# Performance work log

Hardware: AMD Instinct MI355X
Metric: run time of the kernel (lower is better)

Reference implementation:

```python
import jax, jax.numpy as jnp
import numpy as np

H = 1024        # hidden_size
E = 8           # num_experts
K = 2           # experts_per_token
I = 1024        # intermediate_size (mlp1 outputs 2*I, interleaved gate/linear)
N = 4096        # n_tokens
ALPHA = 1.702
LIMIT = 7.0
EPS = 1e-5


def setup_inputs() -> dict:
    key = jax.random.key(0)
    ks = jax.random.split(key, 5)
    x = jax.random.normal(ks[0], (N, H), jnp.float32)
    norm_scale = jnp.ones((H,), jnp.float32)
    gate_w = jax.random.normal(ks[1], (H, E), jnp.float32) * 0.02
    gate_b = jnp.zeros((E,), jnp.float32)
    mlp1_w = jax.random.normal(ks[2], (E, 2 * I, H), jnp.float32) * 0.02
    mlp1_b = jnp.zeros((E, 2 * I), jnp.float32)
    mlp2_w = jax.random.normal(ks[3], (E, H, I), jnp.float32) * 0.02
    mlp2_b = jnp.zeros((E, H), jnp.float32)
    return {"x": x, "norm_scale": norm_scale, "gate_w": gate_w, "gate_b": gate_b,
            "mlp1_w": mlp1_w, "mlp1_b": mlp1_b, "mlp2_w": mlp2_w, "mlp2_b": mlp2_b}


def _swiglu(h):
    # even indices = gate, odd indices = linear (interleaved)
    x_g = jnp.minimum(h[..., ::2], LIMIT)           # clip gate above only
    x_l = jnp.clip(h[..., 1::2], -LIMIT, LIMIT)     # clip linear both sides
    return x_g * jax.nn.sigmoid(ALPHA * x_g) * (x_l + 1.0)


def reference(x, norm_scale, gate_w, gate_b, mlp1_w, mlp1_b, mlp2_w, mlp2_b):
    # RMSNorm (fp32)
    t = x * jax.lax.rsqrt(jnp.mean(x * x, axis=-1, keepdims=True) + EPS) * norm_scale
    # Router: top-k gating with softmax over selected logits
    g = t @ gate_w + gate_b                          # [N, E]
    logits, idx = jax.lax.top_k(g, K)                # [N, K]
    w = jax.nn.softmax(logits, axis=-1)              # [N, K]
    n = x.shape[0]
    # Scatter routing weights into dense combine matrix [N, E]
    # (top_k indices are unique per row, so .set is exact)
    combine = jnp.zeros((n, E), x.dtype).at[jnp.arange(n)[:, None], idx].set(w)
    # Per-expert SwiGLU MLP over all tokens, weighted combine + residual.
    # Loop over the small fixed expert count (E=8); avoids materializing the
    # huge [N, K, 2I, H] gathered-weight tensor from the original gather path.
    out = x
    for e in range(E):
        h1 = _swiglu(t @ mlp1_w[e].T + mlp1_b[e])    # [N, I]
        h2 = h1 @ mlp2_w[e].T + mlp2_b[e]            # [N, H]
        out = out + combine[:, e:e + 1] * h2
    return out
```

## Files before the change

kernel.cpp:

```cpp
#include <hip/hip_runtime.h>
#include <hip/hip_bf16.h>
#include <stdint.h>

#define HDIM 1024
#define NEXP 8
#define TOPK 2
#define IDIM 1024
#define TWO_I 2048
#define ALPHA 1.702f
#define LIMIT 7.0f
#define EPS 1e-5f

#define BM 128
#define BN 128
#define BK 64

typedef __attribute__((ext_vector_type(8))) short bf16x8;
typedef __attribute__((ext_vector_type(4))) float f32x4;

typedef __attribute__((address_space(1))) const uint32_t g_u32;
typedef __attribute__((address_space(3))) uint32_t l_u32;

__device__ __forceinline__ void load_lds16(const void* g, void* l) {
    __builtin_amdgcn_global_load_lds((g_u32*)g, (l_u32*)l, 16, 0, 0);
}

__device__ __forceinline__ ushort f2bf(float f) {
    union { float f; uint32_t u; } v{f};
    uint32_t u = v.u;
    return (ushort)((u + 0x7fffu + ((u >> 16) & 1u)) >> 16);
}

#define WAIT_VM8()  do { asm volatile("s_waitcnt vmcnt(8)" ::: "memory"); \
                         __builtin_amdgcn_sched_barrier(0); } while (0)
#define WAIT_VM0()  do { asm volatile("s_waitcnt vmcnt(0)" ::: "memory"); \
                         __builtin_amdgcn_sched_barrier(0); } while (0)
#define BAR()       do { __builtin_amdgcn_sched_barrier(0); \
                         __builtin_amdgcn_s_barrier(); \
                         __builtin_amdgcn_sched_barrier(0); } while (0)

__global__ __launch_bounds__(256) void k_f32_to_bf16(const float* __restrict__ src,
                                                     ushort* __restrict__ dst, int n4) {
    int i = blockIdx.x * blockDim.x + threadIdx.x;
    int stride = gridDim.x * blockDim.x;
    for (; i < n4; i += stride) {
        float4 v = reinterpret_cast<const float4*>(src)[i];
        ushort4 o;
        o.x = f2bf(v.x); o.y = f2bf(v.y); o.z = f2bf(v.z); o.w = f2bf(v.w);
        reinterpret_cast<ushort4*>(dst)[i] = o;
    }
}

__global__ __launch_bounds__(256) void k_conv_w1(const float* __restrict__ src,
                                                 ushort* __restrict__ dst) {
    const int b = blockIdx.x;
    const int e = b >> 11;
    const int j = b & 2047;
    const int dj = ((j & 1) << 10) | (j >> 1);
    const float4* s = reinterpret_cast<const float4*>(src + (size_t)b * HDIM);
    ushort4* d = reinterpret_cast<ushort4*>(dst + ((size_t)e * TWO_I + dj) * HDIM);
    float4 v = s[threadIdx.x];
    ushort4 o;
    o.x = f2bf(v.x); o.y = f2bf(v.y); o.z = f2bf(v.z); o.w = f2bf(v.w);
    d[threadIdx.x] = o;
}

__global__ __launch_bounds__(256) void k_norm_gate(
    const float* __restrict__ x, const float* __restrict__ scale,
    const float* __restrict__ gw, const float* __restrict__ gb,
    ushort* __restrict__ t_bf, float* __restrict__ route_w,
    int* __restrict__ eidx, int n_tok)
{
    const int tok = blockIdx.x * 4 + (threadIdx.x >> 6);
    if (tok >= n_tok) return;
    const int lane = threadIdx.x & 63;

    const float4* xr = reinterpret_cast<const float4*>(x + (size_t)tok * HDIM);
    const float4* sr = reinterpret_cast<const float4*>(scale);
    float4 xv[4], sv[4];
    #pragma unroll
    for (int j = 0; j < 4; ++j) { xv[j] = xr[lane + 64 * j]; sv[j] = sr[lane + 64 * j]; }

    float ss = 0.f;
    #pragma unroll
    for (int j = 0; j < 4; ++j)
        ss += xv[j].x * xv[j].x + xv[j].y * xv[j].y + xv[j].z * xv[j].z + xv[j].w * xv[j].w;
    #pragma unroll
    for (int off = 1; off < 64; off <<= 1) ss += __shfl_xor(ss, off, 64);
    const float rms = rsqrtf(ss / (float)HDIM + EPS);

    float t[4][4];
    ushort4* tw = reinterpret_cast<ushort4*>(t_bf + (size_t)tok * HDIM);
    #pragma unroll
    for (int j = 0; j < 4; ++j) {
        t[j][0] = xv[j].x * rms * sv[j].x;
        t[j][1] = xv[j].y * rms * sv[j].y;
        t[j][2] = xv[j].z * rms * sv[j].z;
        t[j][3] = xv[j].w * rms * sv[j].w;
        ushort4 o;
        o.x = f2bf(t[j][0]); o.y = f2bf(t[j][1]); o.z = f2bf(t[j][2]); o.w = f2bf(t[j][3]);
        tw[lane + 64 * j] = o;
    }

    float g[NEXP];
    #pragma unroll
    for (int e = 0; e < NEXP; ++e) g[e] = 0.f;
    const float4* gwv = reinterpret_cast<const float4*>(gw);
    #pragma unroll
    for (int j = 0; j < 4; ++j) {
        #pragma unroll
        for (int c = 0; c < 4; ++c) {
            const int h = (lane + 64 * j) * 4 + c;
            const float tv = t[j][c];
            const float4 a = gwv[h * 2 + 0];
            const float4 b = gwv[h * 2 + 1];
            g[0] += tv * a.x; g[1] += tv * a.y; g[2] += tv * a.z; g[3] += tv * a.w;
            g[4] += tv * b.x; g[5] += tv * b.y; g[6] += tv * b.z; g[7] += tv * b.w;
        }
    }
    #pragma unroll
    for (int e = 0; e < NEXP; ++e) {
        #pragma unroll
        for (int off = 1; off < 64; off <<= 1) g[e] += __shfl_xor(g[e], off, 64);
    }

    if (lane == 0) {
        float gg[NEXP];
        #pragma unroll
        for (int e = 0; e < NEXP; ++e) gg[e] = g[e] + gb[e];
        int i0 = 0; float l0 = gg[0];
        #pragma unroll
        for (int e = 1; e < NEXP; ++e) if (gg[e] > l0) { l0 = gg[e]; i0 = e; }
        int i1 = -1; float l1 = -3.4e38f;
        #pragma unroll
        for (int e = 0; e < NEXP; ++e) if (e != i0 && gg[e] > l1) { l1 = gg[e]; i1 = e; }
        const float w0 = 1.f / (1.f + __expf(l1 - l0));
        route_w[tok * 2 + 0] = w0;
        route_w[tok * 2 + 1] = 1.f - w0;
        eidx[tok * 2 + 0] = i0;
        eidx[tok * 2 + 1] = i1;
    }
}

#define BKT_BLOCKS 8
__global__ __launch_bounds__(256) void k_bucket(
    const int* __restrict__ eidx, int* __restrict__ counts,
    int* __restrict__ bucket, int n_tok)
{
    const int total = 2 * n_tok;
    const int per_block = total / BKT_BLOCKS;
    const int rounds = per_block / 256;
    const int base_ent = blockIdx.x * per_block;
    const int tid = threadIdx.x;
    const int lane = tid & 63, wid = tid >> 6;

    __shared__ int wavecnt[4][4][NEXP];
    __shared__ int cum[4][4][NEXP];
    __shared__ int gbase[NEXP];

    int me[4], rank[4];
    #pragma unroll
    for (int r = 0; r < 4; ++r) {
        const int ent = base_ent + r * 256 + tid;
        const int e = (r < rounds) ? eidx[ent] : -1;
        me[r] = e;
        #pragma unroll
        for (int ex = 0; ex < NEXP; ++ex) {
            unsigned long long m = __ballot(e == ex);
            if (e == ex) rank[r] = __popcll(m & ((1ull << lane) - 1ull));
            if (lane == 0) wavecnt[r][wid][ex] = (int)__popcll(m);
        }
    }
    __syncthreads();

    if (tid < 4 * 4 * NEXP) {
        const int e = tid & 7, w = (tid >> 3) & 3, r = tid >> 5;
        int s = 0;
        for (int rr = 0; rr < 4; ++rr)
            for (int ww = 0; ww < 4; ++ww)
                if (rr < r || (rr == r && ww < w)) s += wavecnt[rr][ww][e];
        cum[r][w][e] = s;
    }
    __syncthreads();
    if (tid < NEXP) {
        int tot = 0;
        for (int rr = 0; rr < 4; ++rr)
            for (int ww = 0; ww < 4; ++ww) tot += wavecnt[rr][ww][tid];
        gbase[tid] = atomicAdd(&counts[tid], tot);
    }
    __syncthreads();

    #pragma unroll
    for (int r = 0; r < 4; ++r) {
        const int e = me[r];
        if (e >= 0) {
            const int ent = base_ent + r * 256 + tid;
            bucket[e * n_tok + gbase[e] + cum[r][wid][e] + rank[r]] = ent;
        }
    }
}

__global__ __launch_bounds__(256) void k_gemm1(
    const ushort* __restrict__ tA, const ushort* __restrict__ w1bf,
    const float* __restrict__ b1,
    const int* __restrict__ counts, const int* __restrict__ bucket,
    ushort* __restrict__ h1, int n_tok, int rt_max)
{
    const int bx = blockIdx.x;
    const int rt = bx >> 7;
    const int e  = (bx >> 4) & 7;
    const int jt = bx & 15;
    const int cnt = counts[e];
    if (rt * BM >= cnt) return;

    __shared__ __align__(16) ushort As[2][BM * BK];
    __shared__ __align__(16) ushort Bs[2][BN * BK];

    const int tid = threadIdx.x;
    const int lane = tid & 63, wid = tid >> 6;
    const int wm = wid >> 1, wn = wid & 1;

    int tokrow[4];
    #pragma unroll
    for (int it = 0; it < 4; ++it) {
        int pos = rt * BM + it * 32 + (tid >> 3);
        tokrow[it] = bucket[e * n_tok + min(pos, cnt - 1)] >> 1;
    }
    const ushort* wbase = w1bf + (size_t)e * TWO_I * HDIM;
    const ushort* bsrc[4];
    #pragma unroll
    for (int it = 0; it < 4; ++it) {
        int br = it * 32 + (tid >> 3);
        int G = br >> 4, r16 = br & 15;
        int half = (G >> 1) & 1;
        int sub = ((G >> 2) << 1) | (G & 1);
        int srcrow = half * IDIM + jt * 64 + sub * 16 + r16;
        bsrc[it] = wbase + (size_t)srcrow * HDIM;
    }
    const int swz = (((tid & 7) ^ ((tid >> 3) & 7)) * 8);

    f32x4 acc[4][4];
    #pragma unroll
    for (int mi = 0; mi < 4; ++mi)
        #pragma unroll
        for (int ni = 0; ni < 4; ++ni) acc[mi][ni] = (f32x4)0.f;

    auto stage = [&](int buf, int kt) {
        const int k0 = kt * BK + swz;
        #pragma unroll
        for (int it = 0; it < 4; ++it)
            load_lds16(tA + (size_t)tokrow[it] * HDIM + k0, &As[buf][(it * 32 + wid * 8) * BK]);
        #pragma unroll
        for (int it = 0; it < 4; ++it)
            load_lds16(bsrc[it] + k0, &Bs[buf][(it * 32 + wid * 8) * BK]);
    };
    auto compute = [&](int buf) {
        #pragma unroll
        for (int kk = 0; kk < 2; ++kk) {
            bf16x8 a[4], b[4];
            #pragma unroll
            for (int mi = 0; mi < 4; ++mi) {
                int r = wm * 64 + mi * 16 + (lane & 15);
                int off = r * BK + (((kk * 4 + (lane >> 4)) ^ (lane & 7)) * 8);
                a[mi] = *reinterpret_cast<const bf16x8*>(&As[buf][off]);
            }
            #pragma unroll
            for (int ni = 0; ni < 4; ++ni) {
                int r = wn * 64 + ni * 16 + (lane & 15);
                int off = r * BK + (((kk * 4 + (lane >> 4)) ^ (lane & 7)) * 8);
                b[ni] = *reinterpret_cast<const bf16x8*>(&Bs[buf][off]);
            }
            #pragma unroll
            for (int mi = 0; mi < 4; ++mi)
                #pragma unroll
                for (int ni = 0; ni < 4; ++ni)
                    acc[mi][ni] = __builtin_amdgcn_mfma_f32_16x16x32_bf16(a[mi], b[ni], acc[mi][ni], 0, 0, 0);
        }
    };

    stage(0, 0);
    int cur = 0;
    for (int kt = 0; kt < HDIM / BK - 1; ++kt) {
        stage(cur ^ 1, kt + 1);
        WAIT_VM8();
        BAR();
        compute(cur);
        BAR();
        cur ^= 1;
    }
    WAIT_VM0();
    BAR();
    compute(cur);

    int ent[4][4];
    #pragma unroll
    for (int mi = 0; mi < 4; ++mi)
        #pragma unroll
        for (int r = 0; r < 4; ++r) {
            int pos = rt * BM + wm * 64 + mi * 16 + (lane >> 4) * 4 + r;
            ent[mi][r] = (pos < cnt) ? bucket[e * n_tok + pos] : -1;
        }
    #pragma unroll
    for (int ni = 0; ni < 2; ++ni) {
        const int col = jt * 64 + (wn * 2 + ni) * 16 + (lane & 15);
        const float bg = b1[e * TWO_I + 2 * col];
        const float bl = b1[e * TWO_I + 2 * col + 1];
        #pragma unroll
        for (int mi = 0; mi < 4; ++mi) {
            const f32x4 vg = acc[mi][ni];
            const f32x4 vl = acc[mi][ni + 2];
            #pragma unroll
            for (int r = 0; r < 4; ++r) {
                if (ent[mi][r] >= 0) {
                    const float xg = fminf(vg[r] + bg, LIMIT);
                    const float xl = fminf(fmaxf(vl[r] + bl, -LIMIT), LIMIT);
                    const float s = 1.f / (1.f + __expf(-ALPHA * xg));
                    h1[(size_t)ent[mi][r] * IDIM + col] = f2bf(xg * s * (xl + 1.f));
                }
            }
        }
    }
}

__global__ __launch_bounds__(256) void k_gemm2(
    const ushort* __restrict__ h1, const ushort* __restrict__ w2bf,
    const float* __restrict__ b2, const float* __restrict__ route_w,
    const int* __restrict__ counts, const int* __restrict__ bucket,
    float* __restrict__ contrib, int n_tok, int rt_max)
{
    const int bx = blockIdx.x;
    const int rt = bx >> 6;
    const int e  = (bx >> 3) & 7;
    const int ct = bx & 7;
    const int cnt = counts[e];
    if (rt * BM >= cnt) return;
    const int c0 = ct * BN;

    __shared__ __align__(16) ushort As[2][BM * BK];
    __shared__ __align__(16) ushort Bs[2][BN * BK];

    const int tid = threadIdx.x;
    const int lane = tid & 63, wid = tid >> 6;
    const int wm = wid >> 1, wn = wid & 1;

    int rowent[4];
    #pragma unroll
    for (int it = 0; it < 4; ++it) {
        int pos = rt * BM + it * 32 + (tid >> 3);
        rowent[it] = bucket[e * n_tok + min(pos, cnt - 1)];
    }
    const ushort* wB = w2bf + (size_t)e * HDIM * IDIM;
    const int swz = (((tid & 7) ^ ((tid >> 3) & 7)) * 8);

    f32x4 acc[4][4];
    #pragma unroll
    for (int mi = 0; mi < 4; ++mi)
        #pragma unroll
        for (int ni = 0; ni < 4; ++ni) acc[mi][ni] = (f32x4)0.f;

    auto stage = [&](int buf, int kt) {
        const int k0 = kt * BK + swz;
        #pragma unroll
        for (int it = 0; it < 4; ++it)
            load_lds16(h1 + (size_t)rowent[it] * IDIM + k0, &As[buf][(it * 32 + wid * 8) * BK]);
        #pragma unroll
        for (int it = 0; it < 4; ++it)
            load_lds16(wB + (size_t)(c0 + it * 32 + (tid >> 3)) * IDIM + k0, &Bs[buf][(it * 32 + wid * 8) * BK]);
    };
    auto compute = [&](int buf) {
        #pragma unroll
        for (int kk = 0; kk < 2; ++kk) {
            bf16x8 a[4], b[4];
            #pragma unroll
            for (int mi = 0; mi < 4; ++mi) {
                int r = wm * 64 + mi * 16 + (lane & 15);
                int off = r * BK + (((kk * 4 + (lane >> 4)) ^ (lane & 7)) * 8);
                a[mi] = *reinterpret_cast<const bf16x8*>(&As[buf][off]);
            }
            #pragma unroll
            for (int ni = 0; ni < 4; ++ni) {
                int r = wn * 64 + ni * 16 + (lane & 15);
                int off = r * BK + (((kk * 4 + (lane >> 4)) ^ (lane & 7)) * 8);
                b[ni] = *reinterpret_cast<const bf16x8*>(&Bs[buf][off]);
            }
            #pragma unroll
            for (int mi = 0; mi < 4; ++mi)
                #pragma unroll
                for (int ni = 0; ni < 4; ++ni)
                    acc[mi][ni] = __builtin_amdgcn_mfma_f32_16x16x32_bf16(a[mi], b[ni], acc[mi][ni], 0, 0, 0);
        }
    };

    stage(0, 0);
    int cur = 0;
    for (int kt = 0; kt < IDIM / BK - 1; ++kt) {
        stage(cur ^ 1, kt + 1);
        WAIT_VM8();
        BAR();
        compute(cur);
        BAR();
        cur ^= 1;
    }
    WAIT_VM0();
    BAR();
    compute(cur);

    int ent[4][4];
    float wgt[4][4];
    #pragma unroll
    for (int mi = 0; mi < 4; ++mi)
        #pragma unroll
        for (int r = 0; r < 4; ++r) {
            int pos = rt * BM + wm * 64 + mi * 16 + (lane >> 4) * 4 + r;
            if (pos < cnt) {
                ent[mi][r] = bucket[e * n_tok + pos];
                wgt[mi][r] = route_w[ent[mi][r]];
            } else ent[mi][r] = -1;
        }
    #pragma unroll
    for (int ni = 0; ni < 4; ++ni) {
        const int c = c0 + wn * 64 + ni * 16 + (lane & 15);
        const float bc = b2[e * HDIM + c];
        #pragma unroll
        for (int mi = 0; mi < 4; ++mi) {
            const f32x4 v = acc[mi][ni];
            #pragma unroll
            for (int r = 0; r < 4; ++r) {
                if (ent[mi][r] >= 0) {
                    const int tok = ent[mi][r] >> 1, slot = ent[mi][r] & 1;
                    contrib[((size_t)slot * n_tok + tok) * HDIM + c] = wgt[mi][r] * (v[r] + bc);
                }
            }
        }
    }
}

__global__ __launch_bounds__(256) void k_combine(
    const float* __restrict__ x, const float* __restrict__ contrib,
    float* __restrict__ out, int n4, int slot_stride4)
{
    int i = blockIdx.x * blockDim.x + threadIdx.x;
    if (i >= n4) return;
    float4 xv = reinterpret_cast<const float4*>(x)[i];
    float4 c0 = reinterpret_cast<const float4*>(contrib)[i];
    float4 c1 = reinterpret_cast<const float4*>(contrib)[i + slot_stride4];
    float4 o;
    o.x = xv.x + c0.x + c1.x;
    o.y = xv.y + c0.y + c1.y;
    o.z = xv.z + c0.z + c1.z;
    o.w = xv.w + c0.w + c1.w;
    reinterpret_cast<float4*>(out)[i] = o;
}

extern "C" void kernel_launch(void* const* d_in, const int* in_sizes, int n_in,
                              void* d_out, int out_size, void* d_ws, size_t ws_size,
                              hipStream_t stream) {
    const float* x    = (const float*)d_in[0];
    const float* nsc  = (const float*)d_in[1];
    const float* gw   = (const float*)d_in[2];
    const float* gb   = (const float*)d_in[3];
    const float* w1   = (const float*)d_in[4];
    const float* b1   = (const float*)d_in[5];
    const float* w2   = (const float*)d_in[6];
    const float* b2   = (const float*)d_in[7];
    float* out = (float*)d_out;

    const int N = in_sizes[0] / HDIM;
    const int rt_max = (N + BM - 1) / BM;

    uintptr_t p = (uintptr_t)d_ws;
    auto carve = [&p](size_t bytes) { uintptr_t q = p; p += (bytes + 255) & ~(size_t)255; return q; };
    ushort* t_bf    = (ushort*)carve((size_t)N * HDIM * 2);
    ushort* w1bf    = (ushort*)carve((size_t)NEXP * TWO_I * HDIM * 2);
    ushort* w2bf    = (ushort*)carve((size_t)NEXP * HDIM * IDIM * 2);
    ushort* h1      = (ushort*)carve((size_t)N * TOPK * IDIM * 2);
    float*  contrib = (float*)carve((size_t)TOPK * N * HDIM * 4);
    float*  route_w = (float*)carve((size_t)N * TOPK * 4);
    int*    bucket  = (int*)carve((size_t)NEXP * N * 4);
    int*    eidx    = (int*)carve((size_t)N * TOPK * 4);
    int*    counts  = (int*)carve(256);

    hipMemsetAsync(counts, 0, NEXP * sizeof(int), stream);

    k_conv_w1<<<NEXP * TWO_I, 256, 0, stream>>>(w1, w1bf);
    const int n4w2 = NEXP * HDIM * IDIM / 4;
    k_f32_to_bf16<<<2048, 256, 0, stream>>>(w2, w2bf, n4w2);

    k_norm_gate<<<(N + 3) / 4, 256, 0, stream>>>(x, nsc, gw, gb, t_bf, route_w, eidx, N);
    k_bucket<<<BKT_BLOCKS, 256, 0, stream>>>(eidx, counts, bucket, N);

    k_gemm1<<<rt_max * NEXP * (TWO_I / BN), 256, 0, stream>>>(t_bf, w1bf, b1, counts, bucket, h1, N, rt_max);
    k_gemm2<<<rt_max * NEXP * (HDIM / BN), 256, 0, stream>>>(h1, w2bf, b2, route_w, counts, bucket, contrib, N, rt_max);

    const int n4 = N * HDIM / 4;
    k_combine<<<(n4 + 255) / 256, 256, 0, stream>>>(x, contrib, out, n4, n4);
}
```

Baseline: 328.0 us.

## Enlarge gemm1 tiles to 256x256 with 8 waves and add XCD block swizzle

The first expert GEMM moves from 128x128 tiles with 4 waves to 256x256 tiles with 8 waves per block, which raises arithmetic intensity per LDS load and halves the number of weight and activation reloads. Both expert GEMMs also remap block IDs with an XCD swizzle so that neighbouring tiles sharing the same expert weights land on the same chiplet's L2. The cost is heavier register and LDS use per block (64 KB LDS, 128 accumulator floats per thread), fewer blocks, and more padding waste when per-expert token counts are not multiples of 256.

```diff
diff --git a/kernel.cpp b/kernel.cpp
--- a/kernel.cpp
+++ b/kernel.cpp
@@ -11,8 +11,6 @@
 #define LIMIT 7.0f
 #define EPS 1e-5f
 
-#define BM 128
-#define BN 128
 #define BK 64
 
 typedef __attribute__((ext_vector_type(8))) short bf16x8;
@@ -38,6 +36,11 @@
 #define BAR()       do { __builtin_amdgcn_sched_barrier(0); \
                          __builtin_amdgcn_s_barrier(); \
                          __builtin_amdgcn_sched_barrier(0); } while (0)
+
+__device__ __forceinline__ int xcd_swizzle(int bid, int nwg) {
+    const int cpx = nwg >> 3;
+    return (bid & 7) * cpx + (bid >> 3);
+}
 
 __global__ __launch_bounds__(256) void k_f32_to_bf16(const float* __restrict__ src,
                                                      ushort* __restrict__ dst, int n4) {
@@ -200,48 +203,48 @@
     }
 }
 
-__global__ __launch_bounds__(256) void k_gemm1(
+#define G1_BM 256
+#define G1_BN 256
+__global__ __launch_bounds__(512, 2) void k_gemm1(
     const ushort* __restrict__ tA, const ushort* __restrict__ w1bf,
     const float* __restrict__ b1,
     const int* __restrict__ counts, const int* __restrict__ bucket,
-    ushort* __restrict__ h1, int n_tok, int rt_max)
+    ushort* __restrict__ h1, int n_tok, int nwg)
 {
-    const int bx = blockIdx.x;
-    const int rt = bx >> 7;
-    const int e  = (bx >> 4) & 7;
-    const int jt = bx & 15;
+    const int bx = xcd_swizzle(blockIdx.x, nwg);
+    const int rt = bx >> 6;
+    const int e  = (bx >> 3) & 7;
+    const int jt = bx & 7;
     const int cnt = counts[e];
-    if (rt * BM >= cnt) return;
-
-    __shared__ __align__(16) ushort As[2][BM * BK];
-    __shared__ __align__(16) ushort Bs[2][BN * BK];
+    if (rt * G1_BM >= cnt) return;
+
+    __shared__ __align__(16) ushort As[2][G1_BM * BK];
+    __shared__ __align__(16) ushort Bs[2][G1_BN * BK];
 
     const int tid = threadIdx.x;
     const int lane = tid & 63, wid = tid >> 6;
-    const int wm = wid >> 1, wn = wid & 1;
+    const int wm = wid >> 2, wn = wid & 3;
 
     int tokrow[4];
     #pragma unroll
     for (int it = 0; it < 4; ++it) {
-        int pos = rt * BM + it * 32 + (tid >> 3);
+        int pos = rt * G1_BM + it * 64 + (tid >> 3);
         tokrow[it] = bucket[e * n_tok + min(pos, cnt - 1)] >> 1;
     }
     const ushort* wbase = w1bf + (size_t)e * TWO_I * HDIM;
     const ushort* bsrc[4];
     #pragma unroll
     for (int it = 0; it < 4; ++it) {
-        int br = it * 32 + (tid >> 3);
-        int G = br >> 4, r16 = br & 15;
-        int half = (G >> 1) & 1;
-        int sub = ((G >> 2) << 1) | (G & 1);
-        int srcrow = half * IDIM + jt * 64 + sub * 16 + r16;
+        int br = it * 64 + (tid >> 3);
+        int wnb = br >> 6, q = (br >> 4) & 3, r16 = br & 15;
+        int srcrow = ((q >> 1) ? IDIM : 0) + jt * 128 + wnb * 32 + (q & 1) * 16 + r16;
         bsrc[it] = wbase + (size_t)srcrow * HDIM;
     }
     const int swz = (((tid & 7) ^ ((tid >> 3) & 7)) * 8);
 
-    f32x4 acc[4][4];
-    #pragma unroll
-    for (int mi = 0; mi < 4; ++mi)
+    f32x4 acc[8][4];
+    #pragma unroll
+    for (int mi = 0; mi < 8; ++mi)
         #pragma unroll
         for (int ni = 0; ni < 4; ++ni) acc[mi][ni] = (f32x4)0.f;
 
@@ -249,18 +252,18 @@
         const int k0 = kt * BK + swz;
         #pragma unroll
         for (int it = 0; it < 4; ++it)
-            load_lds16(tA + (size_t)tokrow[it] * HDIM + k0, &As[buf][(it * 32 + wid * 8) * BK]);
+            load_lds16(tA + (size_t)tokrow[it] * HDIM + k0, &As[buf][(it * 64 + wid * 8) * BK]);
         #pragma unroll
         for (int it = 0; it < 4; ++it)
-            load_lds16(bsrc[it] + k0, &Bs[buf][(it * 32 + wid * 8) * BK]);
+            load_lds16(bsrc[it] + k0, &Bs[buf][(it * 64 + wid * 8) * BK]);
     };
     auto compute = [&](int buf) {
         #pragma unroll
         for (int kk = 0; kk < 2; ++kk) {
-            bf16x8 a[4], b[4];
-            #pragma unroll
-            for (int mi = 0; mi < 4; ++mi) {
-                int r = wm * 64 + mi * 16 + (lane & 15);
+            bf16x8 a[8], b[4];
+            #pragma unroll
+            for (int mi = 0; mi < 8; ++mi) {
+                int r = wm * 128 + mi * 16 + (lane & 15);
                 int off = r * BK + (((kk * 4 + (lane >> 4)) ^ (lane & 7)) * 8);
                 a[mi] = *reinterpret_cast<const bf16x8*>(&As[buf][off]);
             }
@@ -271,7 +274,7 @@
                 b[ni] = *reinterpret_cast<const bf16x8*>(&Bs[buf][off]);
             }
             #pragma unroll
-            for (int mi = 0; mi < 4; ++mi)
+            for (int mi = 0; mi < 8; ++mi)
                 #pragma unroll
                 for (int ni = 0; ni < 4; ++ni)
                     acc[mi][ni] = __builtin_amdgcn_mfma_f32_16x16x32_bf16(a[mi], b[ni], acc[mi][ni], 0, 0, 0);
@@ -292,21 +295,21 @@
     BAR();
     compute(cur);
 
-    int ent[4][4];
-    #pragma unroll
-    for (int mi = 0; mi < 4; ++mi)
+    int ent[8][4];
+    #pragma unroll
+    for (int mi = 0; mi < 8; ++mi)
         #pragma unroll
         for (int r = 0; r < 4; ++r) {
-            int pos = rt * BM + wm * 64 + mi * 16 + (lane >> 4) * 4 + r;
+            int pos = rt * G1_BM + wm * 128 + mi * 16 + (lane >> 4) * 4 + r;
             ent[mi][r] = (pos < cnt) ? bucket[e * n_tok + pos] : -1;
         }
     #pragma unroll
     for (int ni = 0; ni < 2; ++ni) {
-        const int col = jt * 64 + (wn * 2 + ni) * 16 + (lane & 15);
-        const float bg = b1[e * TWO_I + 2 * col];
-        const float bl = b1[e * TWO_I + 2 * col + 1];
-        #pragma unroll
-        for (int mi = 0; mi < 4; ++mi) {
+        const int icol = jt * 128 + wn * 32 + ni * 16 + (lane & 15);
+        const float bg = b1[e * TWO_I + 2 * icol];
+        const float bl = b1[e * TWO_I + 2 * icol + 1];
+        #pragma unroll
+        for (int mi = 0; mi < 8; ++mi) {
             const f32x4 vg = acc[mi][ni];
             const f32x4 vl = acc[mi][ni + 2];
             #pragma unroll
@@ -315,20 +318,22 @@
                     const float xg = fminf(vg[r] + bg, LIMIT);
                     const float xl = fminf(fmaxf(vl[r] + bl, -LIMIT), LIMIT);
                     const float s = 1.f / (1.f + __expf(-ALPHA * xg));
-                    h1[(size_t)ent[mi][r] * IDIM + col] = f2bf(xg * s * (xl + 1.f));
+                    h1[(size_t)ent[mi][r] * IDIM + icol] = f2bf(xg * s * (xl + 1.f));
                 }
             }
         }
     }
 }
 
+#define BM 128
+#define BN 128
 __global__ __launch_bounds__(256) void k_gemm2(
     const ushort* __restrict__ h1, const ushort* __restrict__ w2bf,
     const float* __restrict__ b2, const float* __restrict__ route_w,
     const int* __restrict__ counts, const int* __restrict__ bucket,
-    float* __restrict__ contrib, int n_tok, int rt_max)
+    float* __restrict__ contrib, int n_tok, int nwg)
 {
-    const int bx = blockIdx.x;
+    const int bx = xcd_swizzle(blockIdx.x, nwg);
     const int rt = bx >> 6;
     const int e  = (bx >> 3) & 7;
     const int ct = bx & 7;
@@ -466,7 +471,6 @@
     float* out = (float*)d_out;
 
     const int N = in_sizes[0] / HDIM;
-    const int rt_max = (N + BM - 1) / BM;
 
     uintptr_t p = (uintptr_t)d_ws;
     auto carve = [&p](size_t bytes) { uintptr_t q = p; p += (bytes + 255) & ~(size_t)255; return q; };
@@ -489,8 +493,13 @@
     k_norm_gate<<<(N + 3) / 4, 256, 0, stream>>>(x, nsc, gw, gb, t_bf, route_w, eidx, N);
     k_bucket<<<BKT_BLOCKS, 256, 0, stream>>>(eidx, counts, bucket, N);
 
-    k_gemm1<<<rt_max * NEXP * (TWO_I / BN), 256, 0, stream>>>(t_bf, w1bf, b1, counts, bucket, h1, N, rt_max);
-    k_gemm2<<<rt_max * NEXP * (HDIM / BN), 256, 0, stream>>>(h1, w2bf, b2, route_w, counts, bucket, contrib, N, rt_max);
+    const int rt1 = (N + G1_BM - 1) / G1_BM;
+    const int nwg1 = rt1 * NEXP * (TWO_I / G1_BN);
+    k_gemm1<<<nwg1, 512, 0, stream>>>(t_bf, w1bf, b1, counts, bucket, h1, N, nwg1);
+
+    const int rt2 = (N + BM - 1) / BM;
+    const int nwg2 = rt2 * NEXP * (HDIM / BN);
+    k_gemm2<<<nwg2, 256, 0, stream>>>(h1, w2bf, b2, route_w, counts, bucket, contrib, N, nwg2);
 
     const int n4 = N * HDIM / 4;
     k_combine<<<(n4 + 255) / 256, 256, 0, stream>>>(x, contrib, out, n4, n4);
```

New measurement: 508.4 us. 55.0% more time.

## Drop LDS double buffering, raise occupancy, and swizzle blocks across XCDs

Applied to the files above, without the earlier changes.

Both grouped GEMM kernels switch from double-buffered LDS staging to a single buffer with a full vmcnt(0) wait each k-step, halving LDS per block. The launch bounds now request 4 blocks per CU, so more workgroups can be resident to hide latency. Block IDs are remapped so consecutive logical tiles land on the same XCD, which should improve L2 reuse of expert weights. The cost is that loads no longer overlap compute within a block, and the swizzle assumes the grid size is divisible by 8.

```diff
diff --git a/kernel.cpp b/kernel.cpp
--- a/kernel.cpp
+++ b/kernel.cpp
@@ -31,13 +31,16 @@
     return (ushort)((u + 0x7fffu + ((u >> 16) & 1u)) >> 16);
 }
 
-#define WAIT_VM8()  do { asm volatile("s_waitcnt vmcnt(8)" ::: "memory"); \
-                         __builtin_amdgcn_sched_barrier(0); } while (0)
 #define WAIT_VM0()  do { asm volatile("s_waitcnt vmcnt(0)" ::: "memory"); \
                          __builtin_amdgcn_sched_barrier(0); } while (0)
 #define BAR()       do { __builtin_amdgcn_sched_barrier(0); \
                          __builtin_amdgcn_s_barrier(); \
                          __builtin_amdgcn_sched_barrier(0); } while (0)
+
+__device__ __forceinline__ int xcd_swizzle(int bid, int nwg) {
+    const int cpx = nwg >> 3;
+    return (bid & 7) * cpx + (bid >> 3);
+}
 
 __global__ __launch_bounds__(256) void k_f32_to_bf16(const float* __restrict__ src,
                                                      ushort* __restrict__ dst, int n4) {
@@ -200,21 +203,21 @@
     }
 }
 
-__global__ __launch_bounds__(256) void k_gemm1(
+__global__ __launch_bounds__(256, 4) void k_gemm1(
     const ushort* __restrict__ tA, const ushort* __restrict__ w1bf,
     const float* __restrict__ b1,
     const int* __restrict__ counts, const int* __restrict__ bucket,
-    ushort* __restrict__ h1, int n_tok, int rt_max)
+    ushort* __restrict__ h1, int n_tok, int nwg)
 {
-    const int bx = blockIdx.x;
+    const int bx = xcd_swizzle(blockIdx.x, nwg);
     const int rt = bx >> 7;
     const int e  = (bx >> 4) & 7;
     const int jt = bx & 15;
     const int cnt = counts[e];
     if (rt * BM >= cnt) return;
 
-    __shared__ __align__(16) ushort As[2][BM * BK];
-    __shared__ __align__(16) ushort Bs[2][BN * BK];
+    __shared__ __align__(16) ushort As[BM * BK];
+    __shared__ __align__(16) ushort Bs[BN * BK];
 
     const int tid = threadIdx.x;
     const int lane = tid & 63, wid = tid >> 6;
@@ -245,16 +248,16 @@
         #pragma unroll
         for (int ni = 0; ni < 4; ++ni) acc[mi][ni] = (f32x4)0.f;
 
-    auto stage = [&](int buf, int kt) {
+    auto stage = [&](int kt) {
         const int k0 = kt * BK + swz;
         #pragma unroll
         for (int it = 0; it < 4; ++it)
-            load_lds16(tA + (size_t)tokrow[it] * HDIM + k0, &As[buf][(it * 32 + wid * 8) * BK]);
+            load_lds16(tA + (size_t)tokrow[it] * HDIM + k0, &As[(it * 32 + wid * 8) * BK]);
         #pragma unroll
         for (int it = 0; it < 4; ++it)
-            load_lds16(bsrc[it] + k0, &Bs[buf][(it * 32 + wid * 8) * BK]);
+            load_lds16(bsrc[it] + k0, &Bs[(it * 32 + wid * 8) * BK]);
     };
-    auto compute = [&](int buf) {
+    auto compute = [&]() {
         #pragma unroll
         for (int kk = 0; kk < 2; ++kk) {
             bf16x8 a[4], b[4];
@@ -262,13 +265,13 @@
             for (int mi = 0; mi < 4; ++mi) {
                 int r = wm * 64 + mi * 16 + (lane & 15);
                 int off = r * BK + (((kk * 4 + (lane >> 4)) ^ (lane & 7)) * 8);
-                a[mi] = *reinterpret_cast<const bf16x8*>(&As[buf][off]);
+                a[mi] = *reinterpret_cast<const bf16x8*>(&As[off]);
             }
             #pragma unroll
             for (int ni = 0; ni < 4; ++ni) {
                 int r = wn * 64 + ni * 16 + (lane & 15);
                 int off = r * BK + (((kk * 4 + (lane >> 4)) ^ (lane & 7)) * 8);
-                b[ni] = *reinterpret_cast<const bf16x8*>(&Bs[buf][off]);
+                b[ni] = *reinterpret_cast<const bf16x8*>(&Bs[off]);
             }
             #pragma unroll
             for (int mi = 0; mi < 4; ++mi)
@@ -278,19 +281,13 @@
         }
     };
 
-    stage(0, 0);
-    int cur = 0;
-    for (int kt = 0; kt < HDIM / BK - 1; ++kt) {
-        stage(cur ^ 1, kt + 1);
-        WAIT_VM8();
+    for (int kt = 0; kt < HDIM / BK; ++kt) {
+        stage(kt);
+        WAIT_VM0();
         BAR();
-        compute(cur);
+        compute();
         BAR();
-        cur ^= 1;
-    }
-    WAIT_VM0();
-    BAR();
-    compute(cur);
+    }
 
     int ent[4][4];
     #pragma unroll
@@ -322,13 +319,13 @@
     }
 }
 
-__global__ __launch_bounds__(256) void k_gemm2(
+__global__ __launch_bounds__(256, 4) void k_gemm2(
     const ushort* __restrict__ h1, const ushort* __restrict__ w2bf,
     const float* __restrict__ b2, const float* __restrict__ route_w,
     const int* __restrict__ counts, const int* __restrict__ bucket,
-    float* __restrict__ contrib, int n_tok, int rt_max)
+    float* __restrict__ contrib, int n_tok, int nwg)
 {
-    const int bx = blockIdx.x;
+    const int bx = xcd_swizzle(blockIdx.x, nwg);
     const int rt = bx >> 6;
     const int e  = (bx >> 3) & 7;
     const int ct = bx & 7;
@@ -336,8 +333,8 @@
     if (rt * BM >= cnt) return;
     const int c0 = ct * BN;
 
-    __shared__ __align__(16) ushort As[2][BM * BK];
-    __shared__ __align__(16) ushort Bs[2][BN * BK];
+    __shared__ __align__(16) ushort As[BM * BK];
+    __shared__ __align__(16) ushort Bs[BN * BK];
 
     const int tid = threadIdx.x;
     const int lane = tid & 63, wid = tid >> 6;
@@ -358,16 +355,16 @@
         #pragma unroll
         for (int ni = 0; ni < 4; ++ni) acc[mi][ni] = (f32x4)0.f;
 
-    auto stage = [&](int buf, int kt) {
+    auto stage = [&](int kt) {
         const int k0 = kt * BK + swz;
         #pragma unroll
         for (int it = 0; it < 4; ++it)
-            load_lds16(h1 + (size_t)rowent[it] * IDIM + k0, &As[buf][(it * 32 + wid * 8) * BK]);
+            load_lds16(h1 + (size_t)rowent[it] * IDIM + k0, &As[(it * 32 + wid * 8) * BK]);
         #pragma unroll
         for (int it = 0; it < 4; ++it)
-            load_lds16(wB + (size_t)(c0 + it * 32 + (tid >> 3)) * IDIM + k0, &Bs[buf][(it * 32 + wid * 8) * BK]);
+            load_lds16(wB + (size_t)(c0 + it * 32 + (tid >> 3)) * IDIM + k0, &Bs[(it * 32 + wid * 8) * BK]);
     };
-    auto compute = [&](int buf) {
+    auto compute = [&]() {
         #pragma unroll
         for (int kk = 0; kk < 2; ++kk) {
             bf16x8 a[4], b[4];
@@ -375,13 +372,13 @@
             for (int mi = 0; mi < 4; ++mi) {
                 int r = wm * 64 + mi * 16 + (lane & 15);
                 int off = r * BK + (((kk * 4 + (lane >> 4)) ^ (lane & 7)) * 8);
-                a[mi] = *reinterpret_cast<const bf16x8*>(&As[buf][off]);
+                a[mi] = *reinterpret_cast<const bf16x8*>(&As[off]);
             }
             #pragma unroll
             for (int ni = 0; ni < 4; ++ni) {
                 int r = wn * 64 + ni * 16 + (lane & 15);
                 int off = r * BK + (((kk * 4 + (lane >> 4)) ^ (lane & 7)) * 8);
-                b[ni] = *reinterpret_cast<const bf16x8*>(&Bs[buf][off]);
+                b[ni] = *reinterpret_cast<const bf16x8*>(&Bs[off]);
             }
             #pragma unroll
             for (int mi = 0; mi < 4; ++mi)
@@ -391,19 +388,13 @@
         }
     };
 
-    stage(0, 0);
-    int cur = 0;
-    for (int kt = 0; kt < IDIM / BK - 1; ++kt) {
-        stage(cur ^ 1, kt + 1);
-        WAIT_VM8();
+    for (int kt = 0; kt < IDIM / BK; ++kt) {
+        stage(kt);
+        WAIT_VM0();
         BAR();
-        compute(cur);
+        compute();
         BAR();
-        cur ^= 1;
-    }
-    WAIT_VM0();
-    BAR();
-    compute(cur);
+    }
 
     int ent[4][4];
     float wgt[4][4];
@@ -489,8 +480,11 @@
     k_norm_gate<<<(N + 3) / 4, 256, 0, stream>>>(x, nsc, gw, gb, t_bf, route_w, eidx, N);
     k_bucket<<<BKT_BLOCKS, 256, 0, stream>>>(eidx, counts, bucket, N);
 
-    k_gemm1<<<rt_max * NEXP * (TWO_I / BN), 256, 0, stream>>>(t_bf, w1bf, b1, counts, bucket, h1, N, rt_max);
-    k_gemm2<<<rt_max * NEXP * (HDIM / BN), 256, 0, stream>>>(h1, w2bf, b2, route_w, counts, bucket, contrib, N, rt_max);
+    const int nwg1 = rt_max * NEXP * (TWO_I / BN);
+    k_gemm1<<<nwg1, 256, 0, stream>>>(t_bf, w1bf, b1, counts, bucket, h1, N, nwg1);
+
+    const int nwg2 = rt_max * NEXP * (HDIM / BN);
+    k_gemm2<<<nwg2, 256, 0, stream>>>(h1, w2bf, b2, route_w, counts, bucket, contrib, N, nwg2);
 
     const int n4 = N * HDIM / 4;
     k_combine<<<(n4 + 255) / 256, 256, 0, stream>>>(x, contrib, out, n4, n4);
```

Result: slower. 434.1 us (+32.3%).
